# Kernel tuning notes

Hardware: AMD Instinct MI355X
Metric: run time of the kernel (lower is better)

## Reference

```python
import jax, jax.numpy as jnp
import numpy as np

OBS = 128; N_AGENT = 16; N_ACTION = 8; N_LAYER = 2; HID = 128
GE = 256; LE = 256; F1 = 512; F2 = 512


def _edges(batch_size, n):
    # all ordered pairs (i, j), i != j, within each sample; GCNConv adds self-loops
    i, j = np.meshgrid(np.arange(n), np.arange(n), indexing='ij')
    m = i != j
    src0, dst0 = i[m], j[m]                      # [n*(n-1)]
    off = (np.arange(batch_size) * n)[:, None]
    src = (src0[None, :] + off).reshape(-1)
    dst = (dst0[None, :] + off).reshape(-1)
    return jnp.asarray(src, jnp.int32), jnp.asarray(dst, jnp.int32)


def setup_inputs() -> dict:
    key = jax.random.key(0)
    ks = jax.random.split(key, 16)
    g = lambda k, shp, fan: jax.random.normal(k, shp, jnp.float32) / np.sqrt(fan)
    return {
        'obs_j': jax.random.normal(ks[0], (2048, N_AGENT, OBS), jnp.float32),
        'W_pre': g(ks[1], (OBS, HID), OBS), 'b_pre': jnp.zeros((HID,), jnp.float32),
        'W_gcn': g(ks[2], (N_LAYER, HID, HID), HID), 'b_gcn': jnp.zeros((N_LAYER, HID), jnp.float32),
        'W_post': g(ks[3], (HID, GE), HID), 'b_post': jnp.zeros((GE,), jnp.float32),
        'W_loc': g(ks[4], (OBS, LE), OBS), 'b_loc': jnp.zeros((LE,), jnp.float32),
        'W1': g(ks[5], (GE + LE, F1), GE + LE), 'b1': jnp.zeros((F1,), jnp.float32),
        'W2': g(ks[6], (F1, F2), F1), 'b2': jnp.zeros((F2,), jnp.float32),
        'W3': g(ks[7], (F2, N_ACTION), F2), 'b3': jnp.zeros((N_ACTION,), jnp.float32),
    }


def reference(obs_j, W_pre, b_pre, W_gcn, b_gcn, W_post, b_post,
              W_loc, b_loc, W1, b1, W2, b2, W3, b3):
    B, n, _ = obs_j.shape
    N = B * n
    obs = obs_j.reshape(N, OBS)
    x = jax.nn.relu(obs @ W_pre + b_pre)          # [N, HID]

    src, dst = _edges(B, n)
    # GCNConv with self-loops on a fully-connected graph: deg = n for every node,
    # edge norm = 1/sqrt(deg_i*deg_j) = 1/n for every (A+I) edge.
    inv_n = jnp.float32(1.0) / n
    for l in range(N_LAYER):
        h = x @ W_gcn[l]                          # lin (no bias inside propagate)
        agg = jax.ops.segment_sum(h[src], dst, num_segments=N)  # neighbor gather/scatter
        x = jax.nn.relu((agg + h) * inv_n + b_gcn[l])            # + self-loop msg, bias

    g = x.reshape(B, n, HID).mean(axis=1)         # global_mean_pool over each graph
    g = jax.nn.relu(g @ W_post + b_post)          # [B, GE]
    loc = jax.nn.relu(obs @ W_loc + b_loc)        # [B*n, LE]
    gi = jnp.repeat(g, n, axis=0)                 # repeat_interleave over agents
    z = jnp.concatenate([gi, loc], axis=1)
    z = jax.nn.relu(z @ W1 + b1)
    z = jax.nn.relu(z @ W2 + b2)
    q = z @ W3 + b3
    return q.reshape(B, n, N_ACTION)
```

## Files before the change

kernel.cpp:

```cpp
#include <hip/hip_runtime.h>
#include <hip/hip_bf16.h>
#include <stdint.h>

typedef __bf16 bf16;
typedef __bf16 bf16x4 __attribute__((ext_vector_type(4)));
typedef __bf16 bf16x8 __attribute__((ext_vector_type(8)));
typedef float f32x4 __attribute__((ext_vector_type(4)));

#define MFMA(a, b, c) __builtin_amdgcn_mfma_f32_16x16x32_bf16(a, b, c, 0, 0, 0)
#define GL(p) ((const __attribute__((address_space(1))) void*)(p))
#define SH(p) ((__attribute__((address_space(3))) void*)(p))
#define BARRIER() do { __builtin_amdgcn_s_barrier(); asm volatile("" ::: "memory"); } while (0)
#define WAIT_LGKM0() do { asm volatile("s_waitcnt lgkmcnt(0)" ::: "memory"); __builtin_amdgcn_sched_barrier(0); } while (0)
#define WAIT_VM(N) do { asm volatile("s_waitcnt vmcnt(" #N ")" ::: "memory"); __builtin_amdgcn_sched_barrier(0); } while (0)

__device__ inline void tp(const float* W, bf16* WT, int id, int shiftK, int N) {
  int K = 1 << shiftK;
  int n = id >> shiftK;
  int k = id & (K - 1);
  WT[id] = (bf16)W[(size_t)k * N + n];
}

__global__ __launch_bounds__(256) void prep_all(
    const float* __restrict__ Wpre, const float* __restrict__ Wloc,
    const float* __restrict__ Wgcn, const float* __restrict__ Wpost,
    bf16* __restrict__ WpreLocT, bf16* __restrict__ Wg0T, bf16* __restrict__ Wg1T,
    bf16* __restrict__ WpostT,
    const float* __restrict__ bpre, const float* __restrict__ bloc,
    float* __restrict__ biasPL) {
  int blk = blockIdx.x;
  int tid = threadIdx.x;
  if (blk < 448) {
    int id = blk * 256 + tid;
    if (id < 16384) { tp(Wpre, WpreLocT, id, 7, 128); return; } id -= 16384;
    if (id < 32768) { tp(Wloc, WpreLocT + 16384, id, 7, 256); return; } id -= 32768;
    if (id < 16384) { tp(Wgcn, Wg0T, id, 7, 128); return; } id -= 16384;
    if (id < 16384) { tp(Wgcn + 16384, Wg1T, id, 7, 128); return; } id -= 16384;
    tp(Wpost, WpostT, id, 7, 256);
    return;
  }
  if (tid < 128) biasPL[tid] = bpre[tid];
  biasPL[128 + tid] = bloc[tid];
}

__global__ __launch_bounds__(256, 4) void k1c(
    const float* __restrict__ obs, const bf16* __restrict__ WpreLocT,
    const float* __restrict__ biasPL,
    const bf16* __restrict__ Wg0T, const bf16* __restrict__ Wg1T,
    const bf16* __restrict__ WpostT, const float* __restrict__ b_gcn,
    const float* __restrict__ b_post,
    bf16* __restrict__ gB, bf16* __restrict__ loc,
    const float* __restrict__ W1, const float* __restrict__ W2,
    bf16* __restrict__ W1T, bf16* __restrict__ W2T,
    const float* __restrict__ W3, bf16* __restrict__ W3bT,
    float* __restrict__ outq) {
  __shared__ bf16 smem[16384];

  const int tid = threadIdx.x;
  int id = blockIdx.x;

  if (id >= 768) {
    int blk = id - 768;
    if (blk < 128) {
      bf16* tile = smem;
      const float* W = (blk < 64) ? W1 : W2;
      bf16* WT = (blk < 64) ? W1T : W2T;
      int t = blk & 63;
      int tk0 = (t >> 3) * 64, tn0 = (t & 7) * 64;
#pragma unroll
      for (int p = 0; p < 4; p++) {
        int kr = p * 16 + (tid >> 4), nc = (tid & 15) * 4;
        float4 f = *(const float4*)(W + (size_t)(tk0 + kr) * 512 + tn0 + nc);
        bf16x4 v; v[0] = (bf16)f.x; v[1] = (bf16)f.y; v[2] = (bf16)f.z; v[3] = (bf16)f.w;
        *(bf16x4*)&tile[kr * 68 + nc] = v;
      }
      __syncthreads();
#pragma unroll
      for (int p = 0; p < 4; p++) {
        int nr = p * 16 + (tid >> 4), kc = (tid & 15) * 4;
        bf16x4 v;
#pragma unroll
        for (int i = 0; i < 4; i++) v[i] = tile[(kc + i) * 68 + nr];
        *(bf16x4*)(WT + (size_t)(tn0 + nr) * 512 + tk0 + kc) = v;
      }
      return;
    }
    blk -= 128;
    if (blk == 0) {
#pragma unroll
      for (int i = 0; i < 32; i++) {
        int id2 = i * 256 + tid;
        int n = id2 >> 9, k = id2 & 511;
        float w = (n < 8) ? W3[(size_t)k * 8 + n] : 0.f;
        bf16 hi = (bf16)w;
        W3bT[id2] = hi;
        W3bT[8192 + id2] = (bf16)(w - (float)hi);
      }
      return;
    }
    blk -= 1;
    float4 z = {0.f, 0.f, 0.f, 0.f};
#pragma unroll
    for (int i = 0; i < 4; i++)
      ((float4*)outq)[(size_t)blk * 1024 + i * 256 + tid] = z;
    return;
  }

  const int s = id >> 3;
  const int n_idx = s % 3;
  const int m0 = ((id & 7) + 8 * (s / 3)) * 128;
  const int n0 = n_idx * 128;

  f32x4 acc[4][4] = {};
  const int lane = tid & 63, wave = tid >> 6;
  const int wm = (wave >> 1) * 64, wn = (wave & 1) * 64;
  const int lm = lane & 15, quad = lane >> 4;

  float4 pa[4];

  auto loadA = [&](int kt) {
#pragma unroll
    for (int it = 0; it < 2; it++) {
      int idx = it * 256 + tid;
      int row = idx >> 2;
      int c = idx & 3;
      int cv = c ^ ((row >> 1) & 3);
      const float* src = obs + (size_t)(m0 + row) * 128 + kt * 32 + cv * 8;
      pa[it * 2] = *(const float4*)src;
      pa[it * 2 + 1] = *(const float4*)(src + 4);
    }
  };
  auto stageB = [&](int kt, int buf) {
    bf16* Bd = smem + buf * 8192 + 4096;
#pragma unroll
    for (int it = 0; it < 2; it++) {
      int idx = it * 256 + tid;
      int row = idx >> 2;
      int c = idx & 3;
      int cv = c ^ ((row >> 1) & 3);
      const bf16* gb = WpreLocT + (size_t)(n0 + row) * 128 + kt * 32 + cv * 8;
      __builtin_amdgcn_global_load_lds(GL(gb), SH(&Bd[(idx & ~63) * 8]), 16, 0, 0);
    }
  };
  auto commitA = [&](int buf) {
    bf16* Ad = smem + buf * 8192;
#pragma unroll
    for (int it = 0; it < 2; it++) {
      int idx = it * 256 + tid;
      int row = idx >> 2;
      int c = idx & 3;
      float4 f0 = pa[it * 2], f1 = pa[it * 2 + 1];
      bf16x8 v;
      v[0] = (bf16)f0.x; v[1] = (bf16)f0.y; v[2] = (bf16)f0.z; v[3] = (bf16)f0.w;
      v[4] = (bf16)f1.x; v[5] = (bf16)f1.y; v[6] = (bf16)f1.z; v[7] = (bf16)f1.w;
      *(bf16x8*)&Ad[row * 32 + c * 8] = v;
    }
  };
  auto compute = [&](int buf) {
    const bf16* Ar = smem + buf * 8192;
    const bf16* Br = smem + buf * 8192 + 4096;
    bf16x8 a[4], b[4];
#pragma unroll
    for (int i = 0; i < 4; i++) {
      int r = wm + lm + i * 16;
      a[i] = *(const bf16x8*)&Ar[r * 32 + ((quad ^ ((r >> 1) & 3)) * 8)];
    }
#pragma unroll
    for (int j = 0; j < 4; j++) {
      int r = wn + lm + j * 16;
      b[j] = *(const bf16x8*)&Br[r * 32 + ((quad ^ ((r >> 1) & 3)) * 8)];
    }
#pragma unroll
    for (int i = 0; i < 4; i++)
#pragma unroll
      for (int j = 0; j < 4; j++)
        acc[i][j] = MFMA(a[i], b[j], acc[i][j]);
  };

  loadA(0); stageB(0, 0); commitA(0);
  __syncthreads();
#pragma unroll
  for (int i = 0; i < 4; ++i) {
    if (i + 1 < 4) { loadA(i + 1); stageB(i + 1, (i + 1) & 1); }
    compute(i & 1);
    if (i + 1 < 4) commitA((i + 1) & 1);
    __syncthreads();
  }

  if (n_idx == 0) {
    bf16* xs = smem;
    bf16* x2 = smem + 2176;
    bf16* gS = smem + 4352;
#pragma unroll
    for (int i = 0; i < 4; i++) {
      int sl = (wave >> 1) * 4 + i;
#pragma unroll
      for (int j = 0; j < 4; j++) {
        int col = wn + j * 16 + lm;
        float bb = biasPL[col];
        float v = 0.f;
#pragma unroll
        for (int r = 0; r < 4; r++) v += fmaxf(acc[i][j][r] + bb, 0.f);
        v += __shfl_xor(v, 16);
        v += __shfl_xor(v, 32);
        if (quad == 0) xs[sl * 136 + col] = (bf16)(v * 0.0625f);
        else if (quad == 1) xs[(8 + sl) * 136 + col] = (bf16)0.f;
      }
    }
    __syncthreads();
    {
      f32x4 c2[2] = {};
#pragma unroll
      for (int ku = 0; ku < 4; ++ku) {
        bf16x8 a = *(const bf16x8*)&xs[lm * 136 + (ku * 4 + quad) * 8];
#pragma unroll
        for (int jn = 0; jn < 2; ++jn) {
          int col = (wave * 2 + jn) * 16 + lm;
          bf16x8 b = *(const bf16x8*)&Wg0T[(size_t)col * 128 + ku * 32 + quad * 8];
          c2[jn] = MFMA(a, b, c2[jn]);
        }
      }
      __syncthreads();
#pragma unroll
      for (int jn = 0; jn < 2; ++jn) {
        int col = (wave * 2 + jn) * 16 + lm;
        float bb = b_gcn[col];
#pragma unroll
        for (int r = 0; r < 4; ++r)
          x2[(quad * 4 + r) * 136 + col] = (bf16)fmaxf(c2[jn][r] + bb, 0.f);
      }
    }
    __syncthreads();
    {
      f32x4 c2[2] = {};
#pragma unroll
      for (int ku = 0; ku < 4; ++ku) {
        bf16x8 a = *(const bf16x8*)&x2[lm * 136 + (ku * 4 + quad) * 8];
#pragma unroll
        for (int jn = 0; jn < 2; ++jn) {
          int col = (wave * 2 + jn) * 16 + lm;
          bf16x8 b = *(const bf16x8*)&Wg1T[(size_t)col * 128 + ku * 32 + quad * 8];
          c2[jn] = MFMA(a, b, c2[jn]);
        }
      }
      __syncthreads();
#pragma unroll
      for (int jn = 0; jn < 2; ++jn) {
        int col = (wave * 2 + jn) * 16 + lm;
        float bb = b_gcn[128 + col];
#pragma unroll
        for (int r = 0; r < 4; ++r)
          xs[(quad * 4 + r) * 136 + col] = (bf16)fmaxf(c2[jn][r] + bb, 0.f);
      }
    }
    __syncthreads();
    {
      f32x4 c3[4] = {};
#pragma unroll
      for (int ku = 0; ku < 4; ++ku) {
        bf16x8 a = *(const bf16x8*)&xs[lm * 136 + (ku * 4 + quad) * 8];
#pragma unroll
        for (int jn = 0; jn < 4; ++jn) {
          int col = (wave * 4 + jn) * 16 + lm;
          bf16x8 b = *(const bf16x8*)&WpostT[(size_t)col * 128 + ku * 32 + quad * 8];
          c3[jn] = MFMA(a, b, c3[jn]);
        }
      }
#pragma unroll
      for (int jn = 0; jn < 4; ++jn) {
        int col = (wave * 4 + jn) * 16 + lm;
        float bb = b_post[col];
#pragma unroll
        for (int r = 0; r < 4; ++r)
          gS[(quad * 4 + r) * 264 + col] = (bf16)fmaxf(c3[jn][r] + bb, 0.f);
      }
    }
    __syncthreads();
    {
      int sample0 = m0 >> 4;
      int row = tid >> 5, col8 = (tid & 31) * 8;
      *(bf16x8*)&gB[(size_t)(sample0 + row) * 256 + col8] =
          *(const bf16x8*)&gS[row * 264 + col8];
    }
  } else {
#pragma unroll
    for (int i = 0; i < 4; i++)
#pragma unroll
      for (int j = 0; j < 4; j++) {
        int col = wn + j * 16 + lm;
        float bb = biasPL[n0 + col];
#pragma unroll
        for (int r = 0; r < 4; r++) {
          int row = wm + i * 16 + quad * 4 + r;
          smem[row * 128 + col] = (bf16)fmaxf(acc[i][j][r] + bb, 0.f);
        }
      }
    __syncthreads();
    const int coff = n0 - 128;
#pragma unroll
    for (int c = 0; c < 8; c++) {
      int ci = c * 256 + tid;
      int row = ci >> 4, col8 = (ci & 15) * 8;
      *(bf16x8*)&loc[(size_t)(m0 + row) * 256 + coff + col8] = *(const bf16x8*)&smem[row * 128 + col8];
    }
  }
}

__global__ __launch_bounds__(256, 4) void h_k(
    const bf16* __restrict__ gB, const bf16* __restrict__ W1T,
    const float* __restrict__ b1, float* __restrict__ hB) {
  __shared__ bf16 smem[16384];
  const int tid = threadIdx.x;
  const int id = blockIdx.x;
  const int n_idx = id & 3;
  const int m0 = (id >> 2) * 128;
  const int n0 = n_idx * 128;

  f32x4 acc[4][4] = {};
  const int lane = tid & 63, wave = tid >> 6;
  const int wm = (wave >> 1) * 64, wn = (wave & 1) * 64;
  const int lm = lane & 15, quad = lane >> 4;

  auto stage = [&](int kt, int buf) {
    bf16* Ad = smem + buf * 8192;
    bf16* Bd = smem + buf * 8192 + 4096;
    int k0 = kt * 32;
#pragma unroll
    for (int it = 0; it < 2; it++) {
      int idx = it * 256 + tid;
      int row = idx >> 2;
      int c = idx & 3;
      int cv = c ^ ((row >> 1) & 3);
      int kk = k0 + cv * 8;
      const bf16* ga = gB + (size_t)(m0 + row) * 256 + kk;
      __builtin_amdgcn_global_load_lds(GL(ga), SH(&Ad[(idx & ~63) * 8]), 16, 0, 0);
      const bf16* gb = W1T + (size_t)(n0 + row) * 512 + kk;
      __builtin_amdgcn_global_load_lds(GL(gb), SH(&Bd[(idx & ~63) * 8]), 16, 0, 0);
    }
  };
  auto compute = [&](int buf) {
    const bf16* Ar = smem + buf * 8192;
    const bf16* Br = smem + buf * 8192 + 4096;
    bf16x8 a[4], b[4];
#pragma unroll
    for (int i = 0; i < 4; i++) {
      int r = wm + lm + i * 16;
      a[i] = *(const bf16x8*)&Ar[r * 32 + ((quad ^ ((r >> 1) & 3)) * 8)];
    }
#pragma unroll
    for (int j = 0; j < 4; j++) {
      int r = wn + lm + j * 16;
      b[j] = *(const bf16x8*)&Br[r * 32 + ((quad ^ ((r >> 1) & 3)) * 8)];
    }
#pragma unroll
    for (int i = 0; i < 4; i++)
#pragma unroll
      for (int j = 0; j < 4; j++)
        acc[i][j] = MFMA(a[i], b[j], acc[i][j]);
  };

  stage(0, 0);
  __syncthreads();
#pragma unroll 2
  for (int i = 0; i < 8; ++i) {
    if (i + 1 < 8) stage(i + 1, (i + 1) & 1);
    compute(i & 1);
    __syncthreads();
  }

#pragma unroll
  for (int i = 0; i < 4; i++)
#pragma unroll
    for (int j = 0; j < 4; j++) {
      int col = n0 + wn + j * 16 + lm;
      float bb = b1[col];
#pragma unroll
      for (int r = 0; r < 4; r++) {
        int row = m0 + wm + i * 16 + quad * 4 + r;
        hB[(size_t)row * 512 + col] = acc[i][j][r] + bb;
      }
    }
}

template <bool HREP>
__global__ __launch_bounds__(256, 4) void gemm_k(
    const bf16* __restrict__ Ab, const bf16* __restrict__ BT,
    const float* __restrict__ bias, const float* __restrict__ hrep,
    bf16* __restrict__ C,
    const bf16* __restrict__ W3bT, const float* __restrict__ b3,
    float* __restrict__ outq) {
  __shared__ bf16 smem[16384];

  const int tid = threadIdx.x;
  const int id = blockIdx.x;
  const int s = id >> 3;
  const int n_idx = s & 3;
  const int m0 = ((id & 7) + 8 * (s >> 2)) * 128;
  const int n0 = n_idx * 128;

  f32x4 acc[4][4] = {};
  const int lane = tid & 63, wave = tid >> 6;
  const int wm = (wave >> 1) * 64, wn = (wave & 1) * 64;
  const int lm = lane & 15, quad = lane >> 4;

  auto stage = [&](int kt, int buf) {
    bf16* Ad = smem + buf * 8192;
    bf16* Bd = smem + buf * 8192 + 4096;
    int k0 = kt * 32;
#pragma unroll
    for (int it = 0; it < 2; it++) {
      int idx = it * 256 + tid;
      int row = idx >> 2;
      int c = idx & 3;
      int cv = c ^ ((row >> 1) & 3);
      int kk = k0 + cv * 8;
      const bf16* ga = Ab + (size_t)(m0 + row) * 256 + kk;
      __builtin_amdgcn_global_load_lds(GL(ga), SH(&Ad[(idx & ~63) * 8]), 16, 0, 0);
      const bf16* gb = BT + (size_t)(n0 + row) * 512 + 256 + kk;
      __builtin_amdgcn_global_load_lds(GL(gb), SH(&Bd[(idx & ~63) * 8]), 16, 0, 0);
    }
  };

  auto compute = [&](int buf) {
    const bf16* Ar = smem + buf * 8192;
    const bf16* Br = smem + buf * 8192 + 4096;
    bf16x8 a[4], b[4];
#pragma unroll
    for (int i = 0; i < 4; i++) {
      int r = wm + lm + i * 16;
      a[i] = *(const bf16x8*)&Ar[r * 32 + ((quad ^ ((r >> 1) & 3)) * 8)];
    }
#pragma unroll
    for (int j = 0; j < 4; j++) {
      int r = wn + lm + j * 16;
      b[j] = *(const bf16x8*)&Br[r * 32 + ((quad ^ ((r >> 1) & 3)) * 8)];
    }
#pragma unroll
    for (int i = 0; i < 4; i++)
#pragma unroll
      for (int j = 0; j < 4; j++)
        acc[i][j] = MFMA(a[i], b[j], acc[i][j]);
  };

  const int NIT = 8;
  stage(0, 0);
  __syncthreads();
#pragma unroll 2
  for (int i = 0; i < NIT; ++i) {
    if (i + 1 < NIT) stage(i + 1, (i + 1) & 1);
    compute(i & 1);
    __syncthreads();
  }

#pragma unroll
  for (int i = 0; i < 4; i++) {
    int sample = (m0 + wm + i * 16) >> 4;
#pragma unroll
    for (int j = 0; j < 4; j++) {
      int col = n0 + wn + j * 16 + lm;
      float hv = hrep[(size_t)sample * 512 + col];
#pragma unroll
      for (int r = 0; r < 4; r++) {
        int row = wm + i * 16 + quad * 4 + r;
        smem[row * 128 + (col - n0)] = (bf16)fmaxf(acc[i][j][r] + hv, 0.f);
      }
    }
  }
  __syncthreads();
#pragma unroll
  for (int c = 0; c < 8; c++) {
    int ci = c * 256 + tid;
    int row = ci >> 4, col8 = (ci & 15) * 8;
    *(bf16x8*)&C[(size_t)(m0 + row) * 512 + n0 + col8] = *(const bf16x8*)&smem[row * 128 + col8];
  }
}

__global__ __launch_bounds__(512, 1) void k4_8ph(
    const bf16* __restrict__ Ab, const bf16* __restrict__ W2T,
    const float* __restrict__ b2, const bf16* __restrict__ W3bT,
    const float* __restrict__ b3, float* __restrict__ outq) {
  __shared__ bf16 smem[65536];

  const int tid = threadIdx.x;
  const int id = blockIdx.x;
  const int n_idx = id >> 7;
  const int m0 = (id & 127) * 256;
  const int n0 = n_idx * 256;

  f32x4 acc[8][4] = {};
  const int lane = tid & 63, wave = tid >> 6;
  const int wm = (wave >> 2) * 128, wn = (wave & 3) * 64;
  const int lm = lane & 15, quad = lane >> 4;

  auto stageH = [&](int t, int m, int kh, int buf) {
    bf16* D = smem + buf * 32768 + m * 16384 + kh * 8192;
    const bf16* S = m ? W2T : Ab;
    int rbase = m ? n0 : m0;
#pragma unroll
    for (int it = 0; it < 2; it++) {
      int idx = it * 512 + tid;
      int row = idx >> 2;
      int c = idx & 3;
      int cv = c ^ ((row >> 1) & 3);
      const bf16* g = S + (size_t)(rbase + row) * 512 + t * 64 + kh * 32 + cv * 8;
      __builtin_amdgcn_global_load_lds(GL(g), SH(&D[(idx & ~63) * 8]), 16, 0, 0);
    }
  };
  auto dsrA = [&](bf16x8* a, int buf, int ihalf, int kh) {
    const bf16* Ar = smem + buf * 32768 + kh * 8192;
#pragma unroll
    for (int i = 0; i < 4; i++) {
      int r = wm + lm + (ihalf * 4 + i) * 16;
      a[i] = *(const bf16x8*)&Ar[r * 32 + ((quad ^ ((r >> 1) & 3)) * 8)];
    }
  };
  auto dsrB = [&](bf16x8* b, int buf, int kh) {
    const bf16* Br = smem + buf * 32768 + 16384 + kh * 8192;
#pragma unroll
    for (int j = 0; j < 4; j++) {
      int r = wn + lm + j * 16;
      b[j] = *(const bf16x8*)&Br[r * 32 + ((quad ^ ((r >> 1) & 3)) * 8)];
    }
  };
  auto mfma16 = [&](bf16x8* a, bf16x8* b, int ihalf) {
    __builtin_amdgcn_s_setprio(1);
#pragma unroll
    for (int i = 0; i < 4; i++)
#pragma unroll
      for (int j = 0; j < 4; j++)
        acc[ihalf * 4 + i][j] = MFMA(a[i], b[j], acc[ihalf * 4 + i][j]);
    __builtin_amdgcn_s_setprio(0);
  };

  stageH(0, 0, 0, 0); stageH(0, 1, 0, 0); stageH(0, 0, 1, 0); stageH(0, 1, 1, 0);
  WAIT_VM(4);
  BARRIER();

  const int NT = 8;
  for (int t = 0; t < NT - 1; ++t) {
    int cur = t & 1, nxt = cur ^ 1;
    bf16x8 a[4], b[4];
    dsrA(a, cur, 0, 0); dsrB(b, cur, 0);
    stageH(t + 1, 0, 0, nxt);
    BARRIER(); WAIT_LGKM0();
    mfma16(a, b, 0);
    BARRIER();
    dsrA(a, cur, 1, 0);
    stageH(t + 1, 1, 0, nxt);
    WAIT_VM(4);
    BARRIER(); WAIT_LGKM0();
    mfma16(a, b, 1);
    BARRIER();
    dsrA(a, cur, 0, 1); dsrB(b, cur, 1);
    stageH(t + 1, 0, 1, nxt);
    BARRIER(); WAIT_LGKM0();
    mfma16(a, b, 0);
    BARRIER();
    dsrA(a, cur, 1, 1);
    stageH(t + 1, 1, 1, nxt);
    WAIT_VM(4);
    BARRIER(); WAIT_LGKM0();
    mfma16(a, b, 1);
    BARRIER();
  }
  {
    const int cur = (NT - 1) & 1;
    bf16x8 a[4], b[4];
    dsrA(a, cur, 0, 0); dsrB(b, cur, 0);
    BARRIER(); WAIT_LGKM0();
    mfma16(a, b, 0);
    BARRIER();
    dsrA(a, cur, 1, 0);
    WAIT_VM(0);
    BARRIER(); WAIT_LGKM0();
    mfma16(a, b, 1);
    BARRIER();
    dsrA(a, cur, 0, 1); dsrB(b, cur, 1);
    BARRIER(); WAIT_LGKM0();
    mfma16(a, b, 0);
    BARRIER();
    dsrA(a, cur, 1, 1);
    BARRIER(); WAIT_LGKM0();
    mfma16(a, b, 1);
    BARRIER();
  }

  __syncthreads();
#pragma unroll
  for (int i = 0; i < 8; i++)
#pragma unroll
    for (int j = 0; j < 4; j++) {
      int col = wn + j * 16 + lm;
      float bb = b2[n0 + col];
#pragma unroll
      for (int r = 0; r < 4; r++) {
        int row = wm + i * 16 + quad * 4 + r;
        int pc = (col >> 3) ^ (row & 7);
        smem[row * 256 + pc * 8 + (col & 7)] = (bf16)fmaxf(acc[i][j][r] + bb, 0.f);
      }
    }
  __syncthreads();
  bf16x8 w3h[8], w3l[8];
#pragma unroll
  for (int kt = 0; kt < 8; kt++) {
    w3h[kt] = *(const bf16x8*)&W3bT[lm * 512 + n0 + kt * 32 + quad * 8];
    w3l[kt] = *(const bf16x8*)&W3bT[8192 + lm * 512 + n0 + kt * 32 + quad * 8];
  }
  f32x4 qacc[2] = {};
#pragma unroll
  for (int it = 0; it < 2; it++)
#pragma unroll
    for (int kt = 0; kt < 8; kt++) {
      int rr = wave * 32 + it * 16 + lm;
      bf16x8 a = *(const bf16x8*)&smem[rr * 256 + (((kt * 4 + quad) ^ (rr & 7)) * 8)];
      qacc[it] = MFMA(a, w3h[kt], qacc[it]);
      qacc[it] = MFMA(a, w3l[kt], qacc[it]);
    }
  float qb = (n_idx == 0 && lm < 8) ? b3[lm] : 0.f;
  if (lm < 8) {
#pragma unroll
    for (int it = 0; it < 2; it++)
#pragma unroll
      for (int r = 0; r < 4; r++) {
        int row = m0 + wave * 32 + it * 16 + quad * 4 + r;
        atomicAdd(&outq[(size_t)row * 8 + lm], qacc[it][r] + qb);
      }
  }
}

extern "C" void kernel_launch(void* const* d_in, const int* in_sizes, int n_in,
                              void* d_out, int out_size, void* d_ws, size_t ws_size,
                              hipStream_t stream) {
  const float* obs    = (const float*)d_in[0];
  const float* W_pre  = (const float*)d_in[1];
  const float* b_pre  = (const float*)d_in[2];
  const float* W_gcn  = (const float*)d_in[3];
  const float* b_gcn  = (const float*)d_in[4];
  const float* W_post = (const float*)d_in[5];
  const float* b_post = (const float*)d_in[6];
  const float* W_loc  = (const float*)d_in[7];
  const float* b_loc  = (const float*)d_in[8];
  const float* W1     = (const float*)d_in[9];
  const float* b1     = (const float*)d_in[10];
  const float* W2     = (const float*)d_in[11];
  const float* b2     = (const float*)d_in[12];
  const float* W3     = (const float*)d_in[13];
  const float* b3     = (const float*)d_in[14];
  float* out = (float*)d_out;

  char* p = (char*)d_ws;
  auto alloc = [&](size_t bytes) { char* r = p; p += (bytes + 255) & ~(size_t)255; return r; };
  bf16* WpreLocT = (bf16*)alloc(384 * 128 * 2);
  float* biasPL  = (float*)alloc(384 * 4);
  bf16* Wg0T   = (bf16*)alloc(128 * 128 * 2);
  bf16* Wg1T   = (bf16*)alloc(128 * 128 * 2);
  bf16* WpostT = (bf16*)alloc(256 * 128 * 2);
  bf16* W1T    = (bf16*)alloc(512 * 512 * 2);
  bf16* W2T    = (bf16*)alloc(512 * 512 * 2);
  bf16* W3bT   = (bf16*)alloc(2 * 16 * 512 * 2);
  bf16* gB     = (bf16*)alloc((size_t)2048 * 256 * 2);
  bf16* locB   = (bf16*)alloc((size_t)32768 * 256 * 2);
  float* hB    = (float*)alloc((size_t)2048 * 512 * 4);
  bf16* z1B    = (bf16*)alloc((size_t)32768 * 512 * 2);

  prep_all<<<449, 256, 0, stream>>>(W_pre, W_loc, W_gcn, W_post,
                                    WpreLocT, Wg0T, Wg1T, WpostT,
                                    b_pre, b_loc, biasPL);
  k1c<<<961, 256, 0, stream>>>(obs, WpreLocT, biasPL,
                               Wg0T, Wg1T, WpostT, b_gcn, b_post,
                               gB, locB,
                               W1, W2, W1T, W2T, W3, W3bT, out);
  h_k<<<64, 256, 0, stream>>>(gB, W1T, b1, hB);
  gemm_k<true><<<1024, 256, 0, stream>>>(locB, W1T, nullptr, hB, z1B,
                                         nullptr, nullptr, nullptr);
  k4_8ph<<<256, 512, 0, stream>>>(z1B, W2T, b2, W3bT, b3, out);
}
```

Baseline: 148.2 us.

## Replace loc-half W1 GEMM with 256x256 eight-phase pipelined kernel

Replaces the 128x128-tile gemm_k for the loc part of the first FC layer (K=256) with a 256x256-tile, 512-thread kernel. Its schedule interleaves half-tile global-to-LDS loads with MFMA phases using explicit barriers, vmcnt waits and s_setprio, mirroring the existing k4_8ph kernel. Larger tiles cut how often A and B are reloaded, and the phased schedule overlaps loads with compute. The cost is one block per CU, 128 KB of LDS, and only 256 blocks, so latency hiding has to come from the hand-written schedule.

Measured after the change: 151.0 us. Within noise of the previous version (+1.9%).

```diff
diff --git a/kernel.cpp b/kernel.cpp
--- a/kernel.cpp
+++ b/kernel.cpp
@@ -382,96 +382,136 @@
     }
 }
 
-template <bool HREP>
-__global__ __launch_bounds__(256, 4) void gemm_k(
-    const bf16* __restrict__ Ab, const bf16* __restrict__ BT,
-    const float* __restrict__ bias, const float* __restrict__ hrep,
-    bf16* __restrict__ C,
-    const bf16* __restrict__ W3bT, const float* __restrict__ b3,
-    float* __restrict__ outq) {
-  __shared__ bf16 smem[16384];
+__global__ __launch_bounds__(512, 1) void k3_8ph(
+    const bf16* __restrict__ Ab, const bf16* __restrict__ W1T,
+    const float* __restrict__ hrep, bf16* __restrict__ C) {
+  __shared__ bf16 smem[65536];
 
   const int tid = threadIdx.x;
   const int id = blockIdx.x;
-  const int s = id >> 3;
-  const int n_idx = s & 3;
-  const int m0 = ((id & 7) + 8 * (s >> 2)) * 128;
-  const int n0 = n_idx * 128;
-
-  f32x4 acc[4][4] = {};
+  const int n_idx = id >> 7;
+  const int m0 = (id & 127) * 256;
+  const int n0 = n_idx * 256;
+
+  f32x4 acc[8][4] = {};
   const int lane = tid & 63, wave = tid >> 6;
-  const int wm = (wave >> 1) * 64, wn = (wave & 1) * 64;
+  const int wm = (wave >> 2) * 128, wn = (wave & 3) * 64;
   const int lm = lane & 15, quad = lane >> 4;
 
-  auto stage = [&](int kt, int buf) {
-    bf16* Ad = smem + buf * 8192;
-    bf16* Bd = smem + buf * 8192 + 4096;
-    int k0 = kt * 32;
+  auto stageH = [&](int t, int m, int kh, int buf) {
+    bf16* D = smem + buf * 32768 + m * 16384 + kh * 8192;
 #pragma unroll
     for (int it = 0; it < 2; it++) {
-      int idx = it * 256 + tid;
+      int idx = it * 512 + tid;
       int row = idx >> 2;
       int c = idx & 3;
       int cv = c ^ ((row >> 1) & 3);
-      int kk = k0 + cv * 8;
-      const bf16* ga = Ab + (size_t)(m0 + row) * 256 + kk;
-      __builtin_amdgcn_global_load_lds(GL(ga), SH(&Ad[(idx & ~63) * 8]), 16, 0, 0);
-      const bf16* gb = BT + (size_t)(n0 + row) * 512 + 256 + kk;
-      __builtin_amdgcn_global_load_lds(GL(gb), SH(&Bd[(idx & ~63) * 8]), 16, 0, 0);
-    }
-  };
-
-  auto compute = [&](int buf) {
-    const bf16* Ar = smem + buf * 8192;
-    const bf16* Br = smem + buf * 8192 + 4096;
-    bf16x8 a[4], b[4];
+      int kk = t * 64 + kh * 32 + cv * 8;
+      const bf16* g = m ? (W1T + (size_t)(n0 + row) * 512 + 256 + kk)
+                        : (Ab + (size_t)(m0 + row) * 256 + kk);
+      __builtin_amdgcn_global_load_lds(GL(g), SH(&D[(idx & ~63) * 8]), 16, 0, 0);
+    }
+  };
+  auto dsrA = [&](bf16x8* a, int buf, int ihalf, int kh) {
+    const bf16* Ar = smem + buf * 32768 + kh * 8192;
 #pragma unroll
     for (int i = 0; i < 4; i++) {
-      int r = wm + lm + i * 16;
+      int r = wm + lm + (ihalf * 4 + i) * 16;
       a[i] = *(const bf16x8*)&Ar[r * 32 + ((quad ^ ((r >> 1) & 3)) * 8)];
     }
+  };
+  auto dsrB = [&](bf16x8* b, int buf, int kh) {
+    const bf16* Br = smem + buf * 32768 + 16384 + kh * 8192;
 #pragma unroll
     for (int j = 0; j < 4; j++) {
       int r = wn + lm + j * 16;
       b[j] = *(const bf16x8*)&Br[r * 32 + ((quad ^ ((r >> 1) & 3)) * 8)];
     }
+  };
+  auto mfma16 = [&](bf16x8* a, bf16x8* b, int ihalf) {
+    __builtin_amdgcn_s_setprio(1);
 #pragma unroll
     for (int i = 0; i < 4; i++)
 #pragma unroll
       for (int j = 0; j < 4; j++)
-        acc[i][j] = MFMA(a[i], b[j], acc[i][j]);
-  };
-
-  const int NIT = 8;
-  stage(0, 0);
+        acc[ihalf * 4 + i][j] = MFMA(a[i], b[j], acc[ihalf * 4 + i][j]);
+    __builtin_amdgcn_s_setprio(0);
+  };
+
+  stageH(0, 0, 0, 0); stageH(0, 1, 0, 0); stageH(0, 0, 1, 0); stageH(0, 1, 1, 0);
+  WAIT_VM(4);
+  BARRIER();
+
+  const int NT = 4;
+  for (int t = 0; t < NT - 1; ++t) {
+    int cur = t & 1, nxt = cur ^ 1;
+    bf16x8 a[4], b[4];
+    dsrA(a, cur, 0, 0); dsrB(b, cur, 0);
+    stageH(t + 1, 0, 0, nxt);
+    BARRIER(); WAIT_LGKM0();
+    mfma16(a, b, 0);
+    BARRIER();
+    dsrA(a, cur, 1, 0);
+    stageH(t + 1, 1, 0, nxt);
+    WAIT_VM(4);
+    BARRIER(); WAIT_LGKM0();
+    mfma16(a, b, 1);
+    BARRIER();
+    dsrA(a, cur, 0, 1); dsrB(b, cur, 1);
+    stageH(t + 1, 0, 1, nxt);
+    BARRIER(); WAIT_LGKM0();
+    mfma16(a, b, 0);
+    BARRIER();
+    dsrA(a, cur, 1, 1);
+    stageH(t + 1, 1, 1, nxt);
+    WAIT_VM(4);
+    BARRIER(); WAIT_LGKM0();
+    mfma16(a, b, 1);
+    BARRIER();
+  }
+  {
+    const int cur = (NT - 1) & 1;
+    bf16x8 a[4], b[4];
+    dsrA(a, cur, 0, 0); dsrB(b, cur, 0);
+    BARRIER(); WAIT_LGKM0();
+    mfma16(a, b, 0);
+    BARRIER();
+    dsrA(a, cur, 1, 0);
+    WAIT_VM(0);
+    BARRIER(); WAIT_LGKM0();
+    mfma16(a, b, 1);
+    BARRIER();
+    dsrA(a, cur, 0, 1); dsrB(b, cur, 1);
+    BARRIER(); WAIT_LGKM0();
+    mfma16(a, b, 0);
+    BARRIER();
+    dsrA(a, cur, 1, 1);
+    BARRIER(); WAIT_LGKM0();
+    mfma16(a, b, 1);
+    BARRIER();
+  }
+
   __syncthreads();
-#pragma unroll 2
-  for (int i = 0; i < NIT; ++i) {
-    if (i + 1 < NIT) stage(i + 1, (i + 1) & 1);
-    compute(i & 1);
-    __syncthreads();
-  }
-
-#pragma unroll
-  for (int i = 0; i < 4; i++) {
+#pragma unroll
+  for (int i = 0; i < 8; i++) {
     int sample = (m0 + wm + i * 16) >> 4;
 #pragma unroll
     for (int j = 0; j < 4; j++) {
-      int col = n0 + wn + j * 16 + lm;
-      float hv = hrep[(size_t)sample * 512 + col];
+      int col = wn + j * 16 + lm;
+      float hv = hrep[(size_t)sample * 512 + n0 + col];
 #pragma unroll
       for (int r = 0; r < 4; r++) {
         int row = wm + i * 16 + quad * 4 + r;
-        smem[row * 128 + (col - n0)] = (bf16)fmaxf(acc[i][j][r] + hv, 0.f);
+        smem[row * 256 + col] = (bf16)fmaxf(acc[i][j][r] + hv, 0.f);
       }
     }
   }
   __syncthreads();
 #pragma unroll
-  for (int c = 0; c < 8; c++) {
-    int ci = c * 256 + tid;
-    int row = ci >> 4, col8 = (ci & 15) * 8;
-    *(bf16x8*)&C[(size_t)(m0 + row) * 512 + n0 + col8] = *(const bf16x8*)&smem[row * 128 + col8];
+  for (int c = 0; c < 16; c++) {
+    int ci = c * 512 + tid;
+    int row = ci >> 5, col8 = (ci & 31) * 8;
+    *(bf16x8*)&C[(size_t)(m0 + row) * 512 + n0 + col8] = *(const bf16x8*)&smem[row * 256 + col8];
   }
 }
 
@@ -671,7 +711,6 @@
                                gB, locB,
                                W1, W2, W1T, W2T, W3, W3bT, out);
   h_k<<<64, 256, 0, stream>>>(gB, W1T, b1, hB);
-  gemm_k<true><<<1024, 256, 0, stream>>>(locB, W1T, nullptr, hB, z1B,
-                                         nullptr, nullptr, nullptr);
+  k3_8ph<<<256, 512, 0, stream>>>(locB, W1T, hB, z1B);
   k4_8ph<<<256, 512, 0, stream>>>(z1B, W2T, b2, W3bT, b3, out);
 }
```
